# Performance work log

Measured on AMD Instinct MI355X. Metric: run time of the kernel, lower is better.

## Reference

```python
import jax, jax.numpy as jnp
import numpy as np

TEMP = 1.0  # routing_temperature

def _gelu(x):
    return jax.nn.gelu(x, approximate=False)  # torch nn.GELU default (erf)

def setup_inputs() -> dict:
    key = jax.random.key(0)
    ks = jax.random.split(key, 6)
    B, S, D, E, I = 8, 2048, 768, 8, 3072
    H = I // 2
    def xav(k, shape):
        fan_in, fan_out = shape[-2], shape[-1]
        lim = float(np.sqrt(6.0 / (fan_in + fan_out)))
        return jax.random.uniform(k, shape, jnp.float32, -lim, lim)
    return {
        "x":  jax.random.normal(ks[0], (B, S, D), jnp.float32),
        "Wr": xav(ks[1], (D, E)),
        "br": jnp.zeros((E,), jnp.float32),
        "W1": xav(ks[2], (E, D, I)), "b1": jnp.zeros((E, I), jnp.float32),
        "W2": xav(ks[3], (E, I, H)), "b2": jnp.zeros((E, H), jnp.float32),
        "W3": xav(ks[4], (E, H, D)), "b3": jnp.zeros((E, D), jnp.float32),
        "top_k": 2,
    }

def reference(x, Wr, br, W1, b1, W2, b2, W3, b3, top_k):
    B, S, D = x.shape
    E = Wr.shape[1]
    T = B * S
    xt = x.reshape(T, D)                              # flatten tokens
    logits = (xt @ Wr + br) / TEMP                    # [T, E]
    vals, sel = jax.lax.top_k(logits, top_k)          # [T, k]
    w = jax.nn.softmax(vals, axis=-1)                 # softmax over top-k scores
    # dense per-token combine weights (zero for unselected experts)
    combine = jnp.zeros((T, E), x.dtype).at[jnp.arange(T)[:, None], sel].add(w)
    def step(acc, p):
        W1e, b1e, W2e, b2e, W3e, b3e, ce = p
        h = _gelu(xt @ W1e + b1e)                     # [T, I]
        h = _gelu(h @ W2e + b2e)                      # [T, I//2]
        y = h @ W3e + b3e                             # [T, D]
        return acc + ce[:, None] * y, None
    acc0 = jnp.zeros((T, D), x.dtype)
    out, _ = jax.lax.scan(step, acc0, (W1, b1, W2, b2, W3, b3, combine.T))
    return out.reshape(B, S, D)
```

## Files before the change

### kernel.cpp

```cpp
#include <hip/hip_runtime.h>
#include <hip/hip_fp16.h>
#include <cstdint>
#include <cstddef>

#define TK 16384
#define DD 768
#define EE 8
#define II 3072
#define HH 1536

typedef _Float16 half8 __attribute__((ext_vector_type(8)));
typedef float floatx4 __attribute__((ext_vector_type(4)));

typedef const __attribute__((address_space(1))) uint32_t* gptr_t;
typedef __attribute__((address_space(3))) uint32_t* lptr_t;

#define GLOAD_LDS16(gp, lp) __builtin_amdgcn_global_load_lds( \
    (gptr_t)(const void*)(gp), (lptr_t)(void*)(lp), 16, 0, 0)

__device__ __forceinline__ void xcd_swizzle(int& e, int& m, int& n, bool rev) {
  int gx = gridDim.x, gy = gridDim.y;
  int f = (blockIdx.z * gy + blockIdx.y) * gx + blockIdx.x;
  if (rev) f = gx * gy * 8 - 1 - f;
  int xcd = f & 7, idx = f >> 3;
  int chunk = idx / gx, pos = idx - chunk * gx;
  int logical = chunk * (8 * gx) + xcd * gx + pos;
  int mn = gy * gx;
  e = logical / mn;
  int rem = logical - e * mn;
  m = rem / gx;
  n = rem - m * gx;
}

__global__ __launch_bounds__(256)
void cvtT_kernel(const float* __restrict__ in, __half* __restrict__ out,
                 int K, int N) {
  __shared__ float tile[64][65];
  int e = blockIdx.z;
  const float* inp = in + (size_t)e * K * N + (size_t)(blockIdx.y * 64) * N + blockIdx.x * 64;
  __half* outp = out + (size_t)e * K * N + (size_t)(blockIdx.x * 64) * K + blockIdx.y * 64;
  int s = threadIdx.x;
  int tx = s & 15, r0 = s >> 4;
#pragma unroll
  for (int i = 0; i < 4; ++i) {
    int k = r0 + i * 16;
    float4 v = *(const float4*)&inp[(size_t)k * N + tx * 4];
    tile[k][tx * 4 + 0] = v.x;
    tile[k][tx * 4 + 1] = v.y;
    tile[k][tx * 4 + 2] = v.z;
    tile[k][tx * 4 + 3] = v.w;
  }
  __syncthreads();
  int kp = s & 31;
#pragma unroll
  for (int i = 0; i < 8; ++i) {
    int n = (s >> 5) + i * 8;
    __half2 h = __floats2half2_rn(tile[2 * kp][n], tile[2 * kp + 1][n]);
    *(__half2*)&outp[(size_t)n * K + kp * 2] = h;
  }
}

__global__ __launch_bounds__(256)
void router_kernel(const float* __restrict__ x, const float* __restrict__ Wr,
                   const float* __restrict__ br, int* __restrict__ counts,
                   int* __restrict__ sel, float* __restrict__ wTok,
                   __half* __restrict__ xh) {
  __shared__ float wr_s[EE * DD];
  for (int i = threadIdx.x; i < EE * DD; i += 256) {
    int d = i >> 3, e = i & 7;
    wr_s[e * DD + d] = Wr[i];
  }
  __syncthreads();
  int wid = threadIdx.x >> 6, lane = threadIdx.x & 63;
  int t = blockIdx.x * 4 + wid;
  const float* xt = x + (size_t)t * DD;
  float acc[EE];
#pragma unroll
  for (int e = 0; e < EE; ++e) acc[e] = 0.f;
  for (int d = lane; d < DD; d += 64) {
    float xv = xt[d];
#pragma unroll
    for (int e = 0; e < EE; ++e) acc[e] += xv * wr_s[e * DD + d];
  }
#pragma unroll
  for (int off = 32; off > 0; off >>= 1)
#pragma unroll
    for (int e = 0; e < EE; ++e) acc[e] += __shfl_xor(acc[e], off);
  if (lane == 0) {
    float v[EE];
#pragma unroll
    for (int e = 0; e < EE; ++e) v[e] = acc[e] + br[e];
    int i0 = 0;
#pragma unroll
    for (int e = 1; e < EE; ++e) if (v[e] > v[i0]) i0 = e;
    int i1 = (i0 == 0) ? 1 : 0;
#pragma unroll
    for (int e = 0; e < EE; ++e) if (e != i0 && v[e] > v[i1] && e != i1) { if (v[e] > v[i1]) i1 = e; }
    float e1 = __expf(v[i1] - v[i0]);
    float s = 1.f / (1.f + e1);
    sel[2 * t] = i0; sel[2 * t + 1] = i1;
    wTok[2 * t] = s; wTok[2 * t + 1] = e1 * s;
    atomicAdd(&counts[i0], 1);
    atomicAdd(&counts[i1], 1);
  }
  const float4* xr = (const float4*)xt;
  uint2* xo = (uint2*)(xh + (size_t)t * DD);
#pragma unroll
  for (int j = 0; j < 3; ++j) {
    float4 v = xr[lane + j * 64];
    __half2 a = __floats2half2_rn(v.x, v.y);
    __half2 b = __floats2half2_rn(v.z, v.w);
    uint2 p;
    p.x = *(const unsigned int*)&a;
    p.y = *(const unsigned int*)&b;
    xo[lane + j * 64] = p;
  }
}

__global__ void offsets_kernel(const int* __restrict__ counts, int* __restrict__ offsets,
                               int* __restrict__ cursors) {
  if (threadIdx.x == 0) {
    int o = 0;
    for (int e = 0; e < EE; ++e) { offsets[e] = o; cursors[e] = o; o += counts[e]; }
  }
}

__global__ void scatter_kernel(const int* __restrict__ sel, int* __restrict__ cursors,
                               int* __restrict__ idxList, int* __restrict__ posTok) {
  int t = blockIdx.x * 256 + threadIdx.x;
  if (t < TK) {
#pragma unroll
    for (int k = 0; k < 2; ++k) {
      int e = sel[2 * t + k];
      int p = atomicAdd(&cursors[e], 1);
      idxList[p] = t;
      posTok[2 * t + k] = p;
    }
  }
}

template<int KD, int ND, bool GATHER, bool GELU, bool REV>
__device__ __forceinline__
void ffn_body(const __half* __restrict__ A, const __half* __restrict__ Wt,
              const float* __restrict__ Bias, __half* __restrict__ Out,
              const int* __restrict__ counts, const int* __restrict__ offsets,
              const int* __restrict__ idxList) {
  constexpr int NT = KD / 64;
  int e, mblk, nblk;
  xcd_swizzle(e, mblk, nblk, REV);
  const int cnt = counts[e];
  const int m0 = mblk * 256;
  if (cnt == 0 || m0 >= cnt) return;
  const int off = offsets[e];
  const int n0 = nblk * 256;
  const __half* We = Wt + (size_t)e * KD * ND;
  const float* be = Bias + (size_t)e * ND;

  __shared__ __align__(16) __half As[2][256 * 64];
  __shared__ __align__(16) __half Bs[2][256 * 64];

  const int tid = threadIdx.x;
  const int srow = tid >> 3;
  const int swz = ((tid & 7) ^ (srow & 7)) << 3;

  const __half* aptr[4];
  const __half* bptr[4];
#pragma unroll
  for (int q = 0; q < 4; ++q) {
    int gr = m0 + q * 64 + srow;
    if (gr > cnt - 1) gr = cnt - 1;
    size_t arow = GATHER ? (size_t)idxList[off + gr] : (size_t)(off + gr);
    aptr[q] = A + arow * KD + swz;
    bptr[q] = We + (size_t)(n0 + q * 64 + srow) * KD + swz;
  }

#define STAGE_A(BUF, Q, TS) GLOAD_LDS16(aptr[Q] + (TS) * 64, &As[BUF][(Q) * 4096 + tid * 8])
#define STAGE_B(BUF, Q, TS) GLOAD_LDS16(bptr[Q] + (TS) * 64, &Bs[BUF][(Q) * 4096 + tid * 8])

  const int lane = tid & 63, wv = tid >> 6;
  const int wr = wv >> 2, wc = wv & 3;
  const int lrow = lane & 15, lg = lane >> 4;
  const int rowa = wr * 128 + lrow;
  const int rowb = wc * 64 + lrow;
  int aoff[2], boff[2];
#pragma unroll
  for (int kk = 0; kk < 2; ++kk) {
    aoff[kk] = rowa * 64 + (((kk * 4 + lg) ^ (rowa & 7)) << 3);
    boff[kk] = rowb * 64 + (((kk * 4 + lg) ^ (rowb & 7)) << 3);
  }

  floatx4 acc[8][4];
#pragma unroll
  for (int mi = 0; mi < 8; ++mi)
#pragma unroll
    for (int ni = 0; ni < 4; ++ni) acc[mi][ni] = (floatx4){0.f, 0.f, 0.f, 0.f};

#pragma unroll
  for (int q = 0; q < 4; ++q) STAGE_A(0, q, 0);
#pragma unroll
  for (int q = 0; q < 4; ++q) STAGE_B(0, q, 0);
#pragma unroll
  for (int q = 0; q < 4; ++q) STAGE_A(1, q, 1);
  STAGE_B(1, 0, 1);
  STAGE_B(1, 1, 1);
  asm volatile("s_waitcnt vmcnt(6)" ::: "memory");
  __builtin_amdgcn_s_barrier();

#define BAR() __builtin_amdgcn_s_barrier()
#define WLG() do { asm volatile("s_waitcnt lgkmcnt(0)" ::: "memory"); \
                   __builtin_amdgcn_sched_barrier(0); } while (0)
#define P1() __builtin_amdgcn_s_setprio(1)
#define P0() __builtin_amdgcn_s_setprio(0)
#define MMQ(AF, BF, MB, NB) \
  _Pragma("unroll") for (int kk = 0; kk < 2; ++kk) \
  _Pragma("unroll") for (int mi = 0; mi < 4; ++mi) \
  _Pragma("unroll") for (int ni = 0; ni < 2; ++ni) \
    acc[(MB) + mi][(NB) + ni] = __builtin_amdgcn_mfma_f32_16x16x32_f16( \
        AF[mi][kk], BF[ni][kk], acc[(MB) + mi][(NB) + ni], 0, 0, 0);

#define PHASES(CUR, NXT, TT) { \
  const __half* Ac = &As[CUR][0]; \
  const __half* Bc = &Bs[CUR][0]; \
  half8 af[4][2], bf0[2][2], bf1[2][2]; \
   \
  _Pragma("unroll") for (int mi = 0; mi < 4; ++mi) \
  _Pragma("unroll") for (int kk = 0; kk < 2; ++kk) \
    af[mi][kk] = *(const half8*)&Ac[aoff[kk] + mi * 1024]; \
  _Pragma("unroll") for (int ni = 0; ni < 2; ++ni) \
  _Pragma("unroll") for (int kk = 0; kk < 2; ++kk) \
    bf0[ni][kk] = *(const half8*)&Bc[boff[kk] + ni * 1024]; \
  if ((TT) + 1 < NT) { STAGE_B(NXT, 2, (TT) + 1); STAGE_B(NXT, 3, (TT) + 1); } \
  BAR(); WLG(); P1(); MMQ(af, bf0, 0, 0); P0(); BAR(); \
   \
  _Pragma("unroll") for (int ni = 0; ni < 2; ++ni) \
  _Pragma("unroll") for (int kk = 0; kk < 2; ++kk) \
    bf1[ni][kk] = *(const half8*)&Bc[boff[kk] + (ni + 2) * 1024]; \
  if ((TT) + 2 < NT) { STAGE_A(CUR, 0, (TT) + 2); STAGE_A(CUR, 2, (TT) + 2); } \
  BAR(); WLG(); P1(); MMQ(af, bf1, 0, 2); P0(); BAR(); \
   \
  _Pragma("unroll") for (int mi = 0; mi < 4; ++mi) \
  _Pragma("unroll") for (int kk = 0; kk < 2; ++kk) \
    af[mi][kk] = *(const half8*)&Ac[aoff[kk] + (mi + 4) * 1024]; \
  if ((TT) + 2 < NT) { STAGE_B(CUR, 0, (TT) + 2); STAGE_B(CUR, 1, (TT) + 2); } \
  BAR(); WLG(); P1(); MMQ(af, bf0, 4, 0); P0(); BAR(); \
   \
  if ((TT) + 2 < NT) { STAGE_A(CUR, 1, (TT) + 2); STAGE_A(CUR, 3, (TT) + 2); } \
  BAR(); P1(); MMQ(af, bf1, 4, 2); P0(); \
  if ((TT) + 2 < NT) { asm volatile("s_waitcnt vmcnt(6)" ::: "memory"); } \
  else              { asm volatile("s_waitcnt vmcnt(0)" ::: "memory"); } \
  BAR(); }

  for (int t = 0; t < NT; t += 2) {
    PHASES(0, 1, t)
    PHASES(1, 0, t + 1)
  }

  const int crow = m0 + wr * 128 + lg * 4;
  const int ccol = n0 + wc * 64 + lrow;
  float bv[4];
#pragma unroll
  for (int ni = 0; ni < 4; ++ni) bv[ni] = be[ccol + ni * 16];
#pragma unroll
  for (int mi = 0; mi < 8; ++mi) {
#pragma unroll
    for (int j = 0; j < 4; ++j) {
      int r = crow + mi * 16 + j;
      if (r < cnt) {
#pragma unroll
        for (int ni = 0; ni < 4; ++ni) {
          float v = acc[mi][ni][j] + bv[ni];
          if (GELU) v = 0.5f * v * (1.f + erff(v * 0.70710678118654752f));
          Out[(size_t)(off + r) * ND + ccol + ni * 16] = __float2half(v);
        }
      }
    }
  }
#undef STAGE_A
#undef STAGE_B
#undef BAR
#undef WLG
#undef P1
#undef P0
#undef MMQ
#undef PHASES
}

__global__ __launch_bounds__(512, 1)
void ffn_s1(const __half* __restrict__ A, const __half* __restrict__ Wt,
            const float* __restrict__ Bias, __half* __restrict__ Out,
            const int* __restrict__ counts, const int* __restrict__ offsets,
            const int* __restrict__ idxL) {
  ffn_body<DD, II, true, true, false>(A, Wt, Bias, Out, counts, offsets, idxL);
}
__global__ __launch_bounds__(512, 1)
void ffn_s2(const __half* __restrict__ A, const __half* __restrict__ Wt,
            const float* __restrict__ Bias, __half* __restrict__ Out,
            const int* __restrict__ counts, const int* __restrict__ offsets,
            const int* __restrict__ idxL) {
  ffn_body<II, HH, false, true, true>(A, Wt, Bias, Out, counts, offsets, idxL);
}
__global__ __launch_bounds__(512, 1)
void ffn_s3(const __half* __restrict__ A, const __half* __restrict__ Wt,
            const float* __restrict__ Bias, __half* __restrict__ Out,
            const int* __restrict__ counts, const int* __restrict__ offsets,
            const int* __restrict__ idxL) {
  ffn_body<HH, DD, false, false, false>(A, Wt, Bias, Out, counts, offsets, idxL);
}

__global__ void combine_kernel(const __half* __restrict__ yc, const float* __restrict__ wTok,
                               const int* __restrict__ posTok, float* __restrict__ out) {
  int t = blockIdx.x;
  int d = threadIdx.x * 4;
  if (d >= DD) return;
  float w0 = wTok[2 * t], w1 = wTok[2 * t + 1];
  const __half2* a = (const __half2*)(yc + (size_t)posTok[2 * t] * DD + d);
  const __half2* b = (const __half2*)(yc + (size_t)posTok[2 * t + 1] * DD + d);
  float2 a0 = __half22float2(a[0]), a1 = __half22float2(a[1]);
  float2 b0 = __half22float2(b[0]), b1 = __half22float2(b[1]);
  float4 r;
  r.x = w0 * a0.x + w1 * b0.x;
  r.y = w0 * a0.y + w1 * b0.y;
  r.z = w0 * a1.x + w1 * b1.x;
  r.w = w0 * a1.y + w1 * b1.y;
  *(float4*)(out + (size_t)t * DD + d) = r;
}

extern "C" void kernel_launch(void* const* d_in, const int* in_sizes, int n_in,
                              void* d_out, int out_size, void* d_ws, size_t ws_size,
                              hipStream_t stream) {
  const float* x  = (const float*)d_in[0];
  const float* Wr = (const float*)d_in[1];
  const float* br = (const float*)d_in[2];
  const float* W1 = (const float*)d_in[3];
  const float* b1 = (const float*)d_in[4];
  const float* W2 = (const float*)d_in[5];
  const float* b2 = (const float*)d_in[6];
  const float* W3 = (const float*)d_in[7];
  const float* b3 = (const float*)d_in[8];
  float* out = (float*)d_out;

  char* ws = (char*)d_ws;
  size_t o = 0;
  auto alloc = [&](size_t bytes) {
    char* p = ws + o;
    o += (bytes + 255) & ~(size_t)255;
    return p;
  };
  __half* xh   = (__half*)alloc((size_t)TK * DD * 2);
  __half* w1t  = (__half*)alloc((size_t)EE * DD * II * 2);
  __half* w2t  = (__half*)alloc((size_t)EE * II * HH * 2);
  __half* w3t  = (__half*)alloc((size_t)EE * HH * DD * 2);
  __half* h1   = (__half*)alloc((size_t)2 * TK * II * 2);
  __half* h2   = (__half*)alloc((size_t)2 * TK * HH * 2);
  __half* yc   = (__half*)alloc((size_t)2 * TK * DD * 2);
  int*   idxL  = (int*)alloc(2 * TK * 4);
  int*   sel   = (int*)alloc(2 * TK * 4);
  float* wTok  = (float*)alloc(2 * TK * 4);
  int*   posT  = (int*)alloc(2 * TK * 4);
  int*   counts  = (int*)alloc(256);
  int*   offsets = (int*)alloc(256);
  int*   cursors = (int*)alloc(256);
  if (o > ws_size) return;

  hipMemsetAsync(counts, 0, 256, stream);

  cvtT_kernel<<<dim3(II / 64, DD / 64, EE), 256, 0, stream>>>(W1, w1t, DD, II);
  cvtT_kernel<<<dim3(HH / 64, II / 64, EE), 256, 0, stream>>>(W2, w2t, II, HH);
  cvtT_kernel<<<dim3(DD / 64, HH / 64, EE), 256, 0, stream>>>(W3, w3t, HH, DD);
  router_kernel<<<TK / 4, 256, 0, stream>>>(x, Wr, br, counts, sel, wTok, xh);
  offsets_kernel<<<1, 64, 0, stream>>>(counts, offsets, cursors);
  scatter_kernel<<<TK / 256, 256, 0, stream>>>(sel, cursors, idxL, posT);

  ffn_s1<<<dim3(II / 256, 64, EE), 512, 0, stream>>>(xh, w1t, b1, h1, counts, offsets, idxL);
  ffn_s2<<<dim3(HH / 256, 64, EE), 512, 0, stream>>>(h1, w2t, b2, h2, counts, offsets, idxL);
  ffn_s3<<<dim3(DD / 256, 64, EE), 512, 0, stream>>>(h2, w3t, b3, yc, counts, offsets, idxL);

  combine_kernel<<<TK, 192, 0, stream>>>(yc, wTok, posT, out);
}
```

Before: 1.500 ms.

## Replace double-buffered K=64 pipeline with 5/4-stage K=32 ring buffer

Shrinks the K-tile from 64 to 32 and replaces the two-buffer, four-phase schedule with a multi-stage LDS ring (5 slots for A, 4 for B), prefetching 3–4 tiles ahead. Each iteration reads all fragments, issues the next loads, runs 32 MFMAs, then takes a single barrier. The aim is to hide global-load latency through deeper prefetch and to cut the number of barriers per K-step. In exchange it doubles the loop trip count, uses a new LDS swizzle, and the ring offset and vmcnt bookkeeping must be exactly right.

Result: faster. 1.470 ms (-2.0%).

```diff
diff --git a/kernel.cpp b/kernel.cpp
--- a/kernel.cpp
+++ b/kernel.cpp
@@ -145,7 +145,7 @@
               const float* __restrict__ Bias, __half* __restrict__ Out,
               const int* __restrict__ counts, const int* __restrict__ offsets,
               const int* __restrict__ idxList) {
-  constexpr int NT = KD / 64;
+  constexpr int NT = KD / 32;
   int e, mblk, nblk;
   xcd_swizzle(e, mblk, nblk, REV);
   const int cnt = counts[e];
@@ -156,38 +156,35 @@
   const __half* We = Wt + (size_t)e * KD * ND;
   const float* be = Bias + (size_t)e * ND;
 
-  __shared__ __align__(16) __half As[2][256 * 64];
-  __shared__ __align__(16) __half Bs[2][256 * 64];
+  __shared__ __align__(16) __half AsF[5 * 256 * 32];
+  __shared__ __align__(16) __half BsF[4 * 256 * 32];
 
   const int tid = threadIdx.x;
-  const int srow = tid >> 3;
-  const int swz = ((tid & 7) ^ (srow & 7)) << 3;
-
-  const __half* aptr[4];
-  const __half* bptr[4];
-#pragma unroll
-  for (int q = 0; q < 4; ++q) {
-    int gr = m0 + q * 64 + srow;
-    if (gr > cnt - 1) gr = cnt - 1;
+  const int colh = (((tid & 3) ^ ((tid >> 3) & 3)) << 3);
+  const __half* aptr2[2];
+  const __half* bptr2[2];
+#pragma unroll
+  for (int i = 0; i < 2; ++i) {
+    int r = i * 128 + (tid >> 2);
+    int gr = m0 + r; if (gr > cnt - 1) gr = cnt - 1;
     size_t arow = GATHER ? (size_t)idxList[off + gr] : (size_t)(off + gr);
-    aptr[q] = A + arow * KD + swz;
-    bptr[q] = We + (size_t)(n0 + q * 64 + srow) * KD + swz;
-  }
-
-#define STAGE_A(BUF, Q, TS) GLOAD_LDS16(aptr[Q] + (TS) * 64, &As[BUF][(Q) * 4096 + tid * 8])
-#define STAGE_B(BUF, Q, TS) GLOAD_LDS16(bptr[Q] + (TS) * 64, &Bs[BUF][(Q) * 4096 + tid * 8])
+    aptr2[i] = A + arow * KD + colh;
+    bptr2[i] = We + (size_t)(n0 + r) * KD + colh;
+  }
+
+#define STA(WOFF, TS) do { \
+    GLOAD_LDS16(aptr2[0] + (TS) * 32, (char*)AsF + (WOFF) + tid * 16); \
+    GLOAD_LDS16(aptr2[1] + (TS) * 32, (char*)AsF + (WOFF) + tid * 16 + 8192); } while (0)
+#define STB(WOFF, TS) do { \
+    GLOAD_LDS16(bptr2[0] + (TS) * 32, (char*)BsF + (WOFF) + tid * 16); \
+    GLOAD_LDS16(bptr2[1] + (TS) * 32, (char*)BsF + (WOFF) + tid * 16 + 8192); } while (0)
 
   const int lane = tid & 63, wv = tid >> 6;
   const int wr = wv >> 2, wc = wv & 3;
   const int lrow = lane & 15, lg = lane >> 4;
-  const int rowa = wr * 128 + lrow;
-  const int rowb = wc * 64 + lrow;
-  int aoff[2], boff[2];
-#pragma unroll
-  for (int kk = 0; kk < 2; ++kk) {
-    aoff[kk] = rowa * 64 + (((kk * 4 + lg) ^ (rowa & 7)) << 3);
-    boff[kk] = rowb * 64 + (((kk * 4 + lg) ^ (rowb & 7)) << 3);
-  }
+  const int slotSwz = lg ^ ((lrow >> 1) & 3);
+  const int aBase = (wr * 128 + lrow) * 64 + slotSwz * 16;
+  const int bBase = (wc * 64 + lrow) * 64 + slotSwz * 16;
 
   floatx4 acc[8][4];
 #pragma unroll
@@ -195,64 +192,47 @@
 #pragma unroll
     for (int ni = 0; ni < 4; ++ni) acc[mi][ni] = (floatx4){0.f, 0.f, 0.f, 0.f};
 
-#pragma unroll
-  for (int q = 0; q < 4; ++q) STAGE_A(0, q, 0);
-#pragma unroll
-  for (int q = 0; q < 4; ++q) STAGE_B(0, q, 0);
-#pragma unroll
-  for (int q = 0; q < 4; ++q) STAGE_A(1, q, 1);
-  STAGE_B(1, 0, 1);
-  STAGE_B(1, 1, 1);
-  asm volatile("s_waitcnt vmcnt(6)" ::: "memory");
+  STA(0 * 16384, 0);
+  STB(0 * 16384, 0);
+  STA(1 * 16384, 1);
+  STB(1 * 16384, 1);
+  STA(2 * 16384, 2);
+  STB(2 * 16384, 2);
+  STA(3 * 16384, 3);
+  asm volatile("s_waitcnt vmcnt(10)" ::: "memory");
   __builtin_amdgcn_s_barrier();
-
-#define BAR() __builtin_amdgcn_s_barrier()
-#define WLG() do { asm volatile("s_waitcnt lgkmcnt(0)" ::: "memory"); \
-                   __builtin_amdgcn_sched_barrier(0); } while (0)
-#define P1() __builtin_amdgcn_s_setprio(1)
-#define P0() __builtin_amdgcn_s_setprio(0)
-#define MMQ(AF, BF, MB, NB) \
-  _Pragma("unroll") for (int kk = 0; kk < 2; ++kk) \
-  _Pragma("unroll") for (int mi = 0; mi < 4; ++mi) \
-  _Pragma("unroll") for (int ni = 0; ni < 2; ++ni) \
-    acc[(MB) + mi][(NB) + ni] = __builtin_amdgcn_mfma_f32_16x16x32_f16( \
-        AF[mi][kk], BF[ni][kk], acc[(MB) + mi][(NB) + ni], 0, 0, 0);
-
-#define PHASES(CUR, NXT, TT) { \
-  const __half* Ac = &As[CUR][0]; \
-  const __half* Bc = &Bs[CUR][0]; \
-  half8 af[4][2], bf0[2][2], bf1[2][2]; \
-   \
-  _Pragma("unroll") for (int mi = 0; mi < 4; ++mi) \
-  _Pragma("unroll") for (int kk = 0; kk < 2; ++kk) \
-    af[mi][kk] = *(const half8*)&Ac[aoff[kk] + mi * 1024]; \
-  _Pragma("unroll") for (int ni = 0; ni < 2; ++ni) \
-  _Pragma("unroll") for (int kk = 0; kk < 2; ++kk) \
-    bf0[ni][kk] = *(const half8*)&Bc[boff[kk] + ni * 1024]; \
-  if ((TT) + 1 < NT) { STAGE_B(NXT, 2, (TT) + 1); STAGE_B(NXT, 3, (TT) + 1); } \
-  BAR(); WLG(); P1(); MMQ(af, bf0, 0, 0); P0(); BAR(); \
-   \
-  _Pragma("unroll") for (int ni = 0; ni < 2; ++ni) \
-  _Pragma("unroll") for (int kk = 0; kk < 2; ++kk) \
-    bf1[ni][kk] = *(const half8*)&Bc[boff[kk] + (ni + 2) * 1024]; \
-  if ((TT) + 2 < NT) { STAGE_A(CUR, 0, (TT) + 2); STAGE_A(CUR, 2, (TT) + 2); } \
-  BAR(); WLG(); P1(); MMQ(af, bf1, 0, 2); P0(); BAR(); \
-   \
-  _Pragma("unroll") for (int mi = 0; mi < 4; ++mi) \
-  _Pragma("unroll") for (int kk = 0; kk < 2; ++kk) \
-    af[mi][kk] = *(const half8*)&Ac[aoff[kk] + (mi + 4) * 1024]; \
-  if ((TT) + 2 < NT) { STAGE_B(CUR, 0, (TT) + 2); STAGE_B(CUR, 1, (TT) + 2); } \
-  BAR(); WLG(); P1(); MMQ(af, bf0, 4, 0); P0(); BAR(); \
-   \
-  if ((TT) + 2 < NT) { STAGE_A(CUR, 1, (TT) + 2); STAGE_A(CUR, 3, (TT) + 2); } \
-  BAR(); P1(); MMQ(af, bf1, 4, 2); P0(); \
-  if ((TT) + 2 < NT) { asm volatile("s_waitcnt vmcnt(6)" ::: "memory"); } \
-  else              { asm volatile("s_waitcnt vmcnt(0)" ::: "memory"); } \
-  BAR(); }
-
-  for (int t = 0; t < NT; t += 2) {
-    PHASES(0, 1, t)
-    PHASES(1, 0, t + 1)
+  __builtin_amdgcn_sched_barrier(0);
+
+  int rA = 0, wA = 4 * 16384;
+  int rB = 0, wB = 3 * 16384;
+
+#pragma unroll 1
+  for (int t = 0; t < NT; ++t) {
+    half8 af[8], bf[4];
+#pragma unroll
+    for (int mi = 0; mi < 8; ++mi)
+      af[mi] = *(const half8*)((const char*)AsF + rA + aBase + mi * 1024);
+#pragma unroll
+    for (int ni = 0; ni < 4; ++ni)
+      bf[ni] = *(const half8*)((const char*)BsF + rB + bBase + ni * 1024);
+    if (t + 3 < NT) STB(wB, t + 3);
+    if (t + 4 < NT) STA(wA, t + 4);
+    __builtin_amdgcn_s_setprio(1);
+#pragma unroll
+    for (int mi = 0; mi < 8; ++mi)
+#pragma unroll
+      for (int ni = 0; ni < 4; ++ni)
+        acc[mi][ni] = __builtin_amdgcn_mfma_f32_16x16x32_f16(
+            af[mi], bf[ni], acc[mi][ni], 0, 0, 0);
+    __builtin_amdgcn_s_setprio(0);
+    if (t + 4 < NT) { asm volatile("s_waitcnt vmcnt(10)" ::: "memory"); }
+    else            { asm volatile("s_waitcnt vmcnt(0)"  ::: "memory"); }
+    __builtin_amdgcn_s_barrier();
+    __builtin_amdgcn_sched_barrier(0);
+    rA += 16384; if (rA == 5 * 16384) rA = 0;
+    wA += 16384; if (wA == 5 * 16384) wA = 0;
+    rB += 16384; if (rB == 4 * 16384) rB = 0;
+    wB += 16384; if (wB == 4 * 16384) wB = 0;
   }
 
   const int crow = m0 + wr * 128 + lg * 4;
@@ -275,14 +255,8 @@
       }
     }
   }
-#undef STAGE_A
-#undef STAGE_B
-#undef BAR
-#undef WLG
-#undef P1
-#undef P0
-#undef MMQ
-#undef PHASES
+#undef STA
+#undef STB
 }
 
 __global__ __launch_bounds__(512, 1)
```
